# Performance work log

Measured on AMD Instinct MI355X. Metric: run time of the kernel, lower is better.

Reference implementation:

```python
import jax, jax.numpy as jnp
import numpy as np

DIM = 1024
NUM_HEADS = 16
HEAD_DIM = DIM // NUM_HEADS
SCALE = HEAD_DIM ** -0.5


def setup_inputs() -> dict:
    key = jax.random.key(0)
    k1, k2, k3 = jax.random.split(key, 3)
    x = jax.random.normal(k1, (2, 2048, DIM), dtype=jnp.float32)
    # nn.Linear weights: stored as [out, in]; y = x @ W.T
    w_qkv = jax.random.normal(k2, (3 * DIM, DIM), dtype=jnp.float32) * (DIM ** -0.5)
    w_proj = jax.random.normal(k3, (DIM, DIM), dtype=jnp.float32) * (DIM ** -0.5)
    return {"x": x, "w_qkv": w_qkv, "w_proj": w_proj}


def reference(x, w_qkv, w_proj):
    B, L, D = x.shape
    qkv = jnp.einsum("bld,ed->ble", x, w_qkv)  # [B, L, 3*D]
    qkv = qkv.reshape(B, L, 3, NUM_HEADS, HEAD_DIM).transpose(2, 0, 3, 1, 4)
    q, k, v = qkv[0], qkv[1], qkv[2]  # each [B, H, L, hd]
    attn = jnp.einsum("bhqd,bhkd->bhqk", q, k) * SCALE
    attn = jax.nn.softmax(attn, axis=-1)
    out = jnp.einsum("bhqk,bhkd->bhqd", attn, v)  # [B, H, L, hd]
    out = out.transpose(0, 2, 1, 3).reshape(B, L, D)
    return jnp.einsum("bld,ed->ble", out, w_proj)
```

## Files before the change

kernel.cpp:

```cpp
#include <hip/hip_runtime.h>
#include <math.h>
#include <stdint.h>

#define B_ 2
#define L_ 2048
#define D_ 1024
#define H_ 16
#define HD_ 64
#define QSCALE_ 0.1803368801f

typedef __attribute__((ext_vector_type(8))) short short8;
typedef __attribute__((ext_vector_type(4))) short short4v;
typedef __attribute__((ext_vector_type(4))) float float4v;

#if defined(__has_builtin)
#if __has_builtin(__builtin_amdgcn_exp2f)
#define EXP2F(x) __builtin_amdgcn_exp2f(x)
#endif
#endif
#ifndef EXP2F
#define EXP2F(x) exp2f(x)
#endif

__device__ __forceinline__ short f2bf(float f) {
    union { float f; unsigned u; } x; x.f = f;
    unsigned r = x.u + 0x7fffu + ((x.u >> 16) & 1u);
    return (short)(r >> 16);
}

__device__ __forceinline__ unsigned fbits(float f) {
    union { float f; unsigned u; } x; x.f = f;
    return x.u;
}

__device__ __forceinline__ unsigned pk_bf_trunc(float a, float b) {
    return __builtin_amdgcn_perm(fbits(b), fbits(a), 0x07060302u);
}

__device__ __forceinline__ void gl_lds16(const void* g, void* l) {
    __builtin_amdgcn_global_load_lds(
        (const __attribute__((address_space(1))) unsigned int*)g,
        (__attribute__((address_space(3))) unsigned int*)l, 16, 0, 0);
}

__global__ __launch_bounds__(256) void cvt_all(const float* __restrict__ x,
                                               const float* __restrict__ wqkv,
                                               const float* __restrict__ wproj,
                                               short* __restrict__ xb,
                                               short* __restrict__ wqkvb,
                                               short* __restrict__ wprojb) {
    int i = blockIdx.x * 256 + threadIdx.x;
    const float* in;
    short* out;
    int idx;
    if (i < 1048576)      { in = x;     out = xb;     idx = i; }
    else if (i < 1835008) { in = wqkv;  out = wqkvb;  idx = i - 1048576; }
    else                  { in = wproj; out = wprojb; idx = i - 1835008; }
    float4 v = ((const float4*)in)[idx];
    short4v o;
    o.x = f2bf(v.x); o.y = f2bf(v.y); o.z = f2bf(v.z); o.w = f2bf(v.w);
    ((short4v*)out)[idx] = o;
}

__global__ __launch_bounds__(256) void gemm_qkv_bf16(const short* __restrict__ A,
                                                     const short* __restrict__ Bm,
                                                     short* __restrict__ Qb,
                                                     short* __restrict__ Kb,
                                                     short* __restrict__ Vb) {
    __shared__ short smem[16384];
    short* As = smem;
    short* Bs = smem + 8192;
    const int tid = threadIdx.x;
    const int w = tid >> 6, l = tid & 63;
    const int lm = l & 15, q = l >> 4;
    const int bid = blockIdx.x;
    const int xcd = bid & 7;
    const int grp = bid >> 3;
    const int n_tile = xcd + 8 * (grp % 3);
    const int m_tile = grp / 3;
    const int m0 = m_tile * 128, n0 = n_tile * 128;
    const int wm = w >> 1, wn = w & 1;

    float4v acc[4][4];
#pragma unroll
    for (int mt = 0; mt < 4; ++mt)
#pragma unroll
        for (int nt = 0; nt < 4; ++nt) acc[mt][nt] = (float4v){0.f, 0.f, 0.f, 0.f};

    for (int k0 = 0; k0 < 1024; k0 += 64) {
        __syncthreads();
#pragma unroll
        for (int h = 0; h < 2; ++h) {
#pragma unroll
            for (int t = 0; t < 2; ++t) {
                int idx8 = w * 128 + t * 64 + l;
                int row = idx8 >> 2, c8 = idx8 & 3;
                gl_lds16(A  + (size_t)(m0 + row) * 1024 + k0 + h * 32 + c8 * 8,
                         (char*)As + h * 8192 + w * 2048 + t * 1024);
                gl_lds16(Bm + (size_t)(n0 + row) * 1024 + k0 + h * 32 + c8 * 8,
                         (char*)Bs + h * 8192 + w * 2048 + t * 1024);
            }
        }
        __syncthreads();
#pragma unroll
        for (int h = 0; h < 2; ++h) {
            short8 af[4], bfr[4];
#pragma unroll
            for (int mt = 0; mt < 4; ++mt)
                af[mt] = *(const short8*)(As + h * 4096 + (wm * 64 + mt * 16 + lm) * 32 + q * 8);
#pragma unroll
            for (int nt = 0; nt < 4; ++nt)
                bfr[nt] = *(const short8*)(Bs + h * 4096 + (wn * 64 + nt * 16 + lm) * 32 + q * 8);
#pragma unroll
            for (int mt = 0; mt < 4; ++mt)
#pragma unroll
                for (int nt = 0; nt < 4; ++nt)
                    acc[mt][nt] = __builtin_amdgcn_mfma_f32_16x16x32_bf16(af[mt], bfr[nt], acc[mt][nt], 0, 0, 0);
        }
    }

    const int which = n0 >> 10;
    if (which < 2) {
        short* dst = (which == 0) ? Qb : Kb;
        const float sc = (which == 0) ? QSCALE_ : 1.0f;
#pragma unroll
        for (int half = 0; half < 2; ++half) {
            __syncthreads();
            if (wm == half) {
#pragma unroll
                for (int mt = 0; mt < 4; ++mt)
#pragma unroll
                    for (int nt = 0; nt < 4; ++nt)
#pragma unroll
                        for (int r = 0; r < 4; ++r)
                            smem[(mt * 16 + q * 4 + r) * 128 + wn * 64 + nt * 16 + lm] =
                                f2bf(acc[mt][nt][r] * sc);
            }
            __syncthreads();
#pragma unroll
            for (int j = 0; j < 4; ++j) {
                const int x = tid + 256 * j;
                const int row = x >> 4, c = x & 15;
                short8 v = *(const short8*)(smem + row * 128 + c * 8);
                const int m = m0 + half * 64 + row;
                const int b = m >> 11, ll = m & 2047;
                const int n = n0 + c * 8;
                const int hh = (n & 1023) >> 6, d = n & 63;
                *(short8*)(dst + (((size_t)b * H_ + hh) * L_ + ll) * HD_ + d) = v;
            }
        }
    } else {
#pragma unroll
        for (int mt = 0; mt < 4; ++mt) {
            const int m = m0 + wm * 64 + mt * 16 + q * 4;
            const int b = m >> 11, ll = m & 2047;
#pragma unroll
            for (int nt = 0; nt < 4; ++nt) {
                const int n = n0 + wn * 64 + nt * 16 + lm;
                const int h = (n & 1023) >> 6, d = n & 63;
                short4v pk;
                pk.x = f2bf(acc[mt][nt][0]); pk.y = f2bf(acc[mt][nt][1]);
                pk.z = f2bf(acc[mt][nt][2]); pk.w = f2bf(acc[mt][nt][3]);
                *(short4v*)(Vb + (((size_t)b * H_ + h) * HD_ + d) * L_ + ll) = pk;
            }
        }
    }
}

__global__ __launch_bounds__(256) void attn_mfma(const short* __restrict__ Qb,
                                                 const short* __restrict__ Kb,
                                                 const short* __restrict__ Vtg,
                                                 short* __restrict__ Ob) {
    __shared__ short KV[4 * 4096];
    __shared__ short Pt[128 * 72];

    const int tid = threadIdx.x;
    const int w = tid >> 6, l = tid & 63;
    const int lm = l & 15, q = l >> 4;
    const int bid = blockIdx.x;
    const int grp = bid >> 3;
    const int bh = (bid & 7) * 4 + (grp & 3);
    const int qt = grp >> 2;

    const short* Qg = Qb  + ((size_t)bh * L_ + qt * 128) * HD_;
    const short* Kg = Kb  + (size_t)bh * L_ * HD_;
    const short* Vg = Vtg + (size_t)bh * HD_ * L_;

#pragma unroll
    for (int t = 0; t < 4; ++t) {
        int idx = tid + 256 * t;
        int row = idx >> 3, c = idx & 7;
        short8 v = *(const short8*)(Qg + row * 64 + c * 8);
        *(short8*)(Pt + row * 64 + ((c ^ (row & 7)) * 8)) = v;
    }

    const int srow = tid >> 3;
    const int sc   = tid & 7;
    const int koff0 = srow * 64 + ((sc ^ (srow & 7)) * 8);
    const int koff1 = koff0 + 32 * 64;

    {
        short8 ka = *(const short8*)(Kg + (size_t)srow * 64 + sc * 8);
        short8 kb = *(const short8*)(Kg + (size_t)(srow + 32) * 64 + sc * 8);
        short8 va = *(const short8*)(Vg + (size_t)srow * L_ + sc * 8);
        short8 vb = *(const short8*)(Vg + (size_t)(srow + 32) * L_ + sc * 8);
        *(short8*)(KV + koff0) = ka;
        *(short8*)(KV + koff1) = kb;
        *(short8*)(KV + 4096 + koff0) = va;
        *(short8*)(KV + 4096 + koff1) = vb;
    }
    short8 kra = *(const short8*)(Kg + (size_t)(64 + srow) * 64 + sc * 8);
    short8 krb = *(const short8*)(Kg + (size_t)(64 + srow + 32) * 64 + sc * 8);
    short8 vra = *(const short8*)(Vg + (size_t)srow * L_ + 64 + sc * 8);
    short8 vrb = *(const short8*)(Vg + (size_t)(srow + 32) * L_ + 64 + sc * 8);

    __syncthreads();

    short8 qf[2][2];
#pragma unroll
    for (int nq = 0; nq < 2; ++nq)
#pragma unroll
        for (int kh = 0; kh < 2; ++kh) {
            int row = w * 32 + nq * 16 + lm;
            int ch = kh * 4 + q;
            qf[nq][kh] = *(const short8*)(Pt + row * 64 + ((ch ^ (row & 7)) * 8));
        }

    int offA0[4], offA1[4], offV[2][4];
#pragma unroll
    for (int nt = 0; nt < 4; ++nt) {
        const int arow = nt * 16 + lm;
        offA0[nt] = arow * 64 + ((q ^ (arow & 7)) * 8);
        offA1[nt] = arow * 64 + (((4 + q) ^ (arow & 7)) * 8);
#pragma unroll
        for (int kh = 0; kh < 2; ++kh)
            offV[kh][nt] = arow * 64 + (((kh * 4 + q) ^ (arow & 7)) * 8);
    }

    float4v o[4][2];
#pragma unroll
    for (int mt = 0; mt < 4; ++mt)
#pragma unroll
        for (int nq = 0; nq < 2; ++nq) o[mt][nq] = (float4v){0.f, 0.f, 0.f, 0.f};
    float lsum[2] = {0.f, 0.f};

    const int prow = w * 32 + lm;

#pragma unroll 2
    for (int t = 0; t < 32; ++t) {
        const int cur = t & 1;
        short* Kl = KV + cur * 8192;
        short* Vt = Kl + 4096;
        short* Kn = KV + (1 - cur) * 8192;
        short* Vn = Kn + 4096;

        __syncthreads();

        if (t < 31) {
            *(short8*)(Kn + koff0) = kra;
            *(short8*)(Kn + koff1) = krb;
            *(short8*)(Vn + koff0) = vra;
            *(short8*)(Vn + koff1) = vrb;
        }
        if (t < 30) {
            kra = *(const short8*)(Kg + (size_t)((t + 2) * 64 + srow) * 64 + sc * 8);
            krb = *(const short8*)(Kg + (size_t)((t + 2) * 64 + srow + 32) * 64 + sc * 8);
            vra = *(const short8*)(Vg + (size_t)srow * L_ + (t + 2) * 64 + sc * 8);
            vrb = *(const short8*)(Vg + (size_t)(srow + 32) * L_ + (t + 2) * 64 + sc * 8);
        }

        float4v st[4][2];
#pragma unroll
        for (int nt = 0; nt < 4; ++nt) {
            short8 a0 = *(const short8*)(Kl + offA0[nt]);
            short8 a1 = *(const short8*)(Kl + offA1[nt]);
#pragma unroll
            for (int nq = 0; nq < 2; ++nq) {
                float4v z = (float4v){0.f, 0.f, 0.f, 0.f};
                z = __builtin_amdgcn_mfma_f32_16x16x32_bf16(a0, qf[nq][0], z, 0, 0, 0);
                z = __builtin_amdgcn_mfma_f32_16x16x32_bf16(a1, qf[nq][1], z, 0, 0, 0);
                st[nt][nq] = z;
            }
        }

#pragma unroll
        for (int nt = 0; nt < 4; ++nt)
#pragma unroll
            for (int nq = 0; nq < 2; ++nq) {
                const float e0 = EXP2F(st[nt][nq][0]);
                const float e1 = EXP2F(st[nt][nq][1]);
                const float e2 = EXP2F(st[nt][nq][2]);
                const float e3 = EXP2F(st[nt][nq][3]);
                lsum[nq] += (e0 + e1) + (e2 + e3);
                uint2 pk;
                pk.x = pk_bf_trunc(e0, e1);
                pk.y = pk_bf_trunc(e2, e3);
                *(uint2*)(Pt + (prow + nq * 16) * 72 + nt * 16 + q * 4) = pk;
            }

#pragma unroll
        for (int kh = 0; kh < 2; ++kh) {
            short8 pb[2];
#pragma unroll
            for (int nq = 0; nq < 2; ++nq)
                pb[nq] = *(const short8*)(Pt + (prow + nq * 16) * 72 + kh * 32 + q * 8);
#pragma unroll
            for (int mt = 0; mt < 4; ++mt) {
                short8 va = *(const short8*)(Vt + offV[kh][mt]);
#pragma unroll
                for (int nq = 0; nq < 2; ++nq)
                    o[mt][nq] = __builtin_amdgcn_mfma_f32_16x16x32_bf16(va, pb[nq], o[mt][nq], 0, 0, 0);
            }
        }
    }

    float inv[2];
#pragma unroll
    for (int nq = 0; nq < 2; ++nq) {
        float s = lsum[nq];
        s += __shfl_xor(s, 16);
        s += __shfl_xor(s, 32);
        inv[nq] = 1.f / s;
    }
    short* OgBase = Ob + ((size_t)bh * L_ + qt * 128) * HD_;
#pragma unroll
    for (int nq = 0; nq < 2; ++nq) {
        const int qrow = w * 32 + nq * 16 + lm;
#pragma unroll
        for (int mt = 0; mt < 4; ++mt) {
            short4v pk;
            pk.x = f2bf(o[mt][nq][0] * inv[nq]);
            pk.y = f2bf(o[mt][nq][1] * inv[nq]);
            pk.z = f2bf(o[mt][nq][2] * inv[nq]);
            pk.w = f2bf(o[mt][nq][3] * inv[nq]);
            *(short4v*)(OgBase + (size_t)qrow * 64 + mt * 16 + q * 4) = pk;
        }
    }
}

__global__ __launch_bounds__(256) void gemm_proj_bf16(const short* __restrict__ Ob,
                                                      const short* __restrict__ Wp,
                                                      float* __restrict__ out) {
    __shared__ short As[2 * 2048];
    __shared__ short Bs[2 * 4096];
    const int tid = threadIdx.x;
    const int w = tid >> 6, l = tid & 63;
    const int lm = l & 15, q = l >> 4;
    const int bid = blockIdx.x;
    const int m0 = (bid >> 3) * 64, n0 = (bid & 7) * 128;
    const int wm = w & 1, wn = w >> 1;
    const int b = m0 >> 11, l0 = m0 & 2047;

    float4v acc[2][4];
#pragma unroll
    for (int mt = 0; mt < 2; ++mt)
#pragma unroll
        for (int nt = 0; nt < 4; ++nt) acc[mt][nt] = (float4v){0.f, 0.f, 0.f, 0.f};

    for (int k0 = 0; k0 < 1024; k0 += 64) {
        const int hh = k0 >> 6;
        __syncthreads();
#pragma unroll
        for (int h = 0; h < 2; ++h) {
            {
                int idx8 = w * 64 + l;
                int row = idx8 >> 2, c8 = idx8 & 3;
                gl_lds16(Ob + (((size_t)b * H_ + hh) * L_ + l0 + row) * HD_ + h * 32 + c8 * 8,
                         (char*)As + h * 4096 + w * 1024);
            }
#pragma unroll
            for (int t = 0; t < 2; ++t) {
                int idx8 = w * 128 + t * 64 + l;
                int row = idx8 >> 2, c8 = idx8 & 3;
                gl_lds16(Wp + (size_t)(n0 + row) * 1024 + k0 + h * 32 + c8 * 8,
                         (char*)Bs + h * 8192 + w * 2048 + t * 1024);
            }
        }
        __syncthreads();
#pragma unroll
        for (int h = 0; h < 2; ++h) {
            short8 af[2], bfr[4];
#pragma unroll
            for (int mt = 0; mt < 2; ++mt)
                af[mt] = *(const short8*)(As + h * 2048 + (wm * 32 + mt * 16 + lm) * 32 + q * 8);
#pragma unroll
            for (int nt = 0; nt < 4; ++nt)
                bfr[nt] = *(const short8*)(Bs + h * 4096 + (wn * 64 + nt * 16 + lm) * 32 + q * 8);
#pragma unroll
            for (int mt = 0; mt < 2; ++mt)
#pragma unroll
                for (int nt = 0; nt < 4; ++nt)
                    acc[mt][nt] = __builtin_amdgcn_mfma_f32_16x16x32_bf16(af[mt], bfr[nt], acc[mt][nt], 0, 0, 0);
        }
    }

#pragma unroll
    for (int mt = 0; mt < 2; ++mt)
#pragma unroll
        for (int nt = 0; nt < 4; ++nt)
#pragma unroll
            for (int r = 0; r < 4; ++r) {
                const int m = m0 + wm * 32 + mt * 16 + q * 4 + r;
                const int n = n0 + wn * 64 + nt * 16 + lm;
                out[(size_t)m * 1024 + n] = acc[mt][nt][r];
            }
}

extern "C" void kernel_launch(void* const* d_in, const int* in_sizes, int n_in,
                              void* d_out, int out_size, void* d_ws, size_t ws_size,
                              hipStream_t stream) {
    (void)in_sizes; (void)n_in; (void)out_size; (void)ws_size;
    const float* x      = (const float*)d_in[0];
    const float* w_qkv  = (const float*)d_in[1];
    const float* w_proj = (const float*)d_in[2];

    char* ws = (char*)d_ws;
    short* xb     = (short*)(ws);
    short* wqkvb  = (short*)(ws + (8u  << 20));
    short* wprojb = (short*)(ws + (14u << 20));
    short* Qb     = (short*)(ws + (16u << 20));
    short* Kb     = (short*)(ws + (24u << 20));
    short* Vb     = (short*)(ws + (32u << 20));
    short* Ob     = (short*)(ws + (40u << 20));

    cvt_all<<<8192, 256, 0, stream>>>(x, w_qkv, w_proj, xb, wqkvb, wprojb);
    gemm_qkv_bf16 <<<768, 256, 0, stream>>>(xb, wqkvb, Qb, Kb, Vb);
    attn_mfma     <<<512, 256, 0, stream>>>(Qb, Kb, Vb, Ob);
    gemm_proj_bf16<<<512, 256, 0, stream>>>(Ob, wprojb, (float*)d_out);
}
```

Before: 192.4 us.

## Register-prefetch double-buffered LDS pipeline in QKV and projection GEMMs

Both GEMM kernels now load global tiles into registers one step ahead and store them into a ping-pong LDS buffer, replacing the direct global-to-LDS loads and the two barriers per iteration. Each iteration handles a K-slice of 32 with a single barrier. This overlaps global memory latency with MFMA compute and removes one barrier per step. The cost is more registers and a VGPR round trip in place of the direct LDS DMA path.

```diff
diff --git a/kernel.cpp b/kernel.cpp
--- a/kernel.cpp
+++ b/kernel.cpp
@@ -35,12 +35,6 @@
 
 __device__ __forceinline__ unsigned pk_bf_trunc(float a, float b) {
     return __builtin_amdgcn_perm(fbits(b), fbits(a), 0x07060302u);
-}
-
-__device__ __forceinline__ void gl_lds16(const void* g, void* l) {
-    __builtin_amdgcn_global_load_lds(
-        (const __attribute__((address_space(1))) unsigned int*)g,
-        (__attribute__((address_space(3))) unsigned int*)l, 16, 0, 0);
 }
 
 __global__ __launch_bounds__(256) void cvt_all(const float* __restrict__ x,
@@ -68,8 +62,6 @@
                                                      short* __restrict__ Kb,
                                                      short* __restrict__ Vb) {
     __shared__ short smem[16384];
-    short* As = smem;
-    short* Bs = smem + 8192;
     const int tid = threadIdx.x;
     const int w = tid >> 6, l = tid & 63;
     const int lm = l & 15, q = l >> 4;
@@ -81,42 +73,69 @@
     const int m0 = m_tile * 128, n0 = n_tile * 128;
     const int wm = w >> 1, wn = w & 1;
 
+    const int srow = tid >> 2;
+    const int sc8  = (tid & 3) * 8;
+    const int soff0 = srow * 32 + sc8;
+    const int soff1 = soff0 + 64 * 32;
+    const short* Ag = A  + (size_t)(m0 + srow) * 1024 + sc8;
+    const short* Bg = Bm + (size_t)(n0 + srow) * 1024 + sc8;
+
     float4v acc[4][4];
 #pragma unroll
     for (int mt = 0; mt < 4; ++mt)
 #pragma unroll
         for (int nt = 0; nt < 4; ++nt) acc[mt][nt] = (float4v){0.f, 0.f, 0.f, 0.f};
 
-    for (int k0 = 0; k0 < 1024; k0 += 64) {
+    {
+        short8 a0 = *(const short8*)(Ag);
+        short8 a1 = *(const short8*)(Ag + 64 * 1024);
+        short8 b0 = *(const short8*)(Bg);
+        short8 b1 = *(const short8*)(Bg + 64 * 1024);
+        *(short8*)(smem + soff0) = a0;
+        *(short8*)(smem + soff1) = a1;
+        *(short8*)(smem + 8192 + soff0) = b0;
+        *(short8*)(smem + 8192 + soff1) = b1;
+    }
+    short8 ar0 = *(const short8*)(Ag + 32);
+    short8 ar1 = *(const short8*)(Ag + 64 * 1024 + 32);
+    short8 br0 = *(const short8*)(Bg + 32);
+    short8 br1 = *(const short8*)(Bg + 64 * 1024 + 32);
+
+    for (int t = 0; t < 32; ++t) {
+        const int cur = t & 1;
+        short* Asc = smem + cur * 4096;
+        short* Asn = smem + (1 - cur) * 4096;
+        short* Bsc = smem + 8192 + cur * 4096;
+        short* Bsn = smem + 8192 + (1 - cur) * 4096;
+
         __syncthreads();
-#pragma unroll
-        for (int h = 0; h < 2; ++h) {
-#pragma unroll
-            for (int t = 0; t < 2; ++t) {
-                int idx8 = w * 128 + t * 64 + l;
-                int row = idx8 >> 2, c8 = idx8 & 3;
-                gl_lds16(A  + (size_t)(m0 + row) * 1024 + k0 + h * 32 + c8 * 8,
-                         (char*)As + h * 8192 + w * 2048 + t * 1024);
-                gl_lds16(Bm + (size_t)(n0 + row) * 1024 + k0 + h * 32 + c8 * 8,
-                         (char*)Bs + h * 8192 + w * 2048 + t * 1024);
-            }
-        }
-        __syncthreads();
-#pragma unroll
-        for (int h = 0; h < 2; ++h) {
-            short8 af[4], bfr[4];
-#pragma unroll
-            for (int mt = 0; mt < 4; ++mt)
-                af[mt] = *(const short8*)(As + h * 4096 + (wm * 64 + mt * 16 + lm) * 32 + q * 8);
+
+        if (t < 31) {
+            *(short8*)(Asn + soff0) = ar0;
+            *(short8*)(Asn + soff1) = ar1;
+            *(short8*)(Bsn + soff0) = br0;
+            *(short8*)(Bsn + soff1) = br1;
+        }
+        if (t < 30) {
+            const int k0 = (t + 2) * 32;
+            ar0 = *(const short8*)(Ag + k0);
+            ar1 = *(const short8*)(Ag + 64 * 1024 + k0);
+            br0 = *(const short8*)(Bg + k0);
+            br1 = *(const short8*)(Bg + 64 * 1024 + k0);
+        }
+
+        short8 af[4], bfr[4];
+#pragma unroll
+        for (int mt = 0; mt < 4; ++mt)
+            af[mt] = *(const short8*)(Asc + (wm * 64 + mt * 16 + lm) * 32 + q * 8);
+#pragma unroll
+        for (int nt = 0; nt < 4; ++nt)
+            bfr[nt] = *(const short8*)(Bsc + (wn * 64 + nt * 16 + lm) * 32 + q * 8);
+#pragma unroll
+        for (int mt = 0; mt < 4; ++mt)
 #pragma unroll
             for (int nt = 0; nt < 4; ++nt)
-                bfr[nt] = *(const short8*)(Bs + h * 4096 + (wn * 64 + nt * 16 + lm) * 32 + q * 8);
-#pragma unroll
-            for (int mt = 0; mt < 4; ++mt)
-#pragma unroll
-                for (int nt = 0; nt < 4; ++nt)
-                    acc[mt][nt] = __builtin_amdgcn_mfma_f32_16x16x32_bf16(af[mt], bfr[nt], acc[mt][nt], 0, 0, 0);
-        }
+                acc[mt][nt] = __builtin_amdgcn_mfma_f32_16x16x32_bf16(af[mt], bfr[nt], acc[mt][nt], 0, 0, 0);
     }
 
     const int which = n0 >> 10;
@@ -351,47 +370,66 @@
     const int wm = w & 1, wn = w >> 1;
     const int b = m0 >> 11, l0 = m0 & 2047;
 
+    const int srow = tid >> 2;
+    const int sc8  = (tid & 3) * 8;
+    const int aoff = srow * 32 + sc8;
+    const int boff0 = aoff;
+    const int boff1 = aoff + 64 * 32;
+    const short* Agb = Ob + (((size_t)b * H_) * L_ + l0 + srow) * HD_;
+    const short* Bg  = Wp + (size_t)(n0 + srow) * 1024 + sc8;
+
     float4v acc[2][4];
 #pragma unroll
     for (int mt = 0; mt < 2; ++mt)
 #pragma unroll
         for (int nt = 0; nt < 4; ++nt) acc[mt][nt] = (float4v){0.f, 0.f, 0.f, 0.f};
 
-    for (int k0 = 0; k0 < 1024; k0 += 64) {
-        const int hh = k0 >> 6;
+    {
+        short8 a0 = *(const short8*)(Agb + sc8);
+        short8 b0 = *(const short8*)(Bg);
+        short8 b1 = *(const short8*)(Bg + 64 * 1024);
+        *(short8*)(As + aoff) = a0;
+        *(short8*)(Bs + boff0) = b0;
+        *(short8*)(Bs + boff1) = b1;
+    }
+    short8 arx = *(const short8*)(Agb + 32 + sc8);
+    short8 brx0 = *(const short8*)(Bg + 32);
+    short8 brx1 = *(const short8*)(Bg + 64 * 1024 + 32);
+
+    for (int t = 0; t < 32; ++t) {
+        const int cur = t & 1;
+        short* Asc = As + cur * 2048;
+        short* Asn = As + (1 - cur) * 2048;
+        short* Bsc = Bs + cur * 4096;
+        short* Bsn = Bs + (1 - cur) * 4096;
+
         __syncthreads();
-#pragma unroll
-        for (int h = 0; h < 2; ++h) {
-            {
-                int idx8 = w * 64 + l;
-                int row = idx8 >> 2, c8 = idx8 & 3;
-                gl_lds16(Ob + (((size_t)b * H_ + hh) * L_ + l0 + row) * HD_ + h * 32 + c8 * 8,
-                         (char*)As + h * 4096 + w * 1024);
-            }
-#pragma unroll
-            for (int t = 0; t < 2; ++t) {
-                int idx8 = w * 128 + t * 64 + l;
-                int row = idx8 >> 2, c8 = idx8 & 3;
-                gl_lds16(Wp + (size_t)(n0 + row) * 1024 + k0 + h * 32 + c8 * 8,
-                         (char*)Bs + h * 8192 + w * 2048 + t * 1024);
-            }
-        }
-        __syncthreads();
-#pragma unroll
-        for (int h = 0; h < 2; ++h) {
-            short8 af[2], bfr[4];
-#pragma unroll
-            for (int mt = 0; mt < 2; ++mt)
-                af[mt] = *(const short8*)(As + h * 2048 + (wm * 32 + mt * 16 + lm) * 32 + q * 8);
+
+        if (t < 31) {
+            *(short8*)(Asn + aoff) = arx;
+            *(short8*)(Bsn + boff0) = brx0;
+            *(short8*)(Bsn + boff1) = brx1;
+        }
+        if (t < 30) {
+            const int tn = t + 2;
+            const int hh = tn >> 1, d = (tn & 1) * 32 + sc8;
+            arx  = *(const short8*)(Agb + (size_t)hh * L_ * HD_ + d);
+            brx0 = *(const short8*)(Bg + tn * 32);
+            brx1 = *(const short8*)(Bg + 64 * 1024 + tn * 32);
+        }
+
+        short8 af[2], bfr[4];
+#pragma unroll
+        for (int mt = 0; mt < 2; ++mt)
+            af[mt] = *(const short8*)(Asc + (wm * 32 + mt * 16 + lm) * 32 + q * 8);
+#pragma unroll
+        for (int nt = 0; nt < 4; ++nt)
+            bfr[nt] = *(const short8*)(Bsc + (wn * 64 + nt * 16 + lm) * 32 + q * 8);
+#pragma unroll
+        for (int mt = 0; mt < 2; ++mt)
 #pragma unroll
             for (int nt = 0; nt < 4; ++nt)
-                bfr[nt] = *(const short8*)(Bs + h * 4096 + (wn * 64 + nt * 16 + lm) * 32 + q * 8);
-#pragma unroll
-            for (int mt = 0; mt < 2; ++mt)
-#pragma unroll
-                for (int nt = 0; nt < 4; ++nt)
-                    acc[mt][nt] = __builtin_amdgcn_mfma_f32_16x16x32_bf16(af[mt], bfr[nt], acc[mt][nt], 0, 0, 0);
-        }
+                acc[mt][nt] = __builtin_amdgcn_mfma_f32_16x16x32_bf16(af[mt], bfr[nt], acc[mt][nt], 0, 0, 0);
     }
 
 #pragma unroll
```

New measurement: 182.9 us. 4.9% less time.
